# Performance work log

Hardware: AMD Instinct MI355X
Metric: run time of the kernel (lower is better)

Reference implementation:

```python
import jax, jax.numpy as jnp
import numpy as np

B = 64; IMG = 224; P = 16; CIN = 3
DM = 192; DEPTH = 24; DSTATE = 16; DINNER = 384; DTR = 12; DCONV = 4
N = (IMG // P) ** 2  # 196 tokens


def setup_inputs() -> dict:
    key = jax.random.key(0)
    ks = jax.random.split(key, 10)
    s = 0.02
    img = jax.random.normal(ks[0], (B, CIN, IMG, IMG), jnp.float32)
    patch_w = jax.random.normal(ks[1], (DM, CIN, P, P), jnp.float32) * s
    patch_b = jnp.zeros((DM,), jnp.float32)
    # per-layer Mamba params, stacked along depth
    in_proj_w = jax.random.normal(ks[2], (DEPTH, 2 * DINNER, DM), jnp.float32) * s
    conv_w = jax.random.normal(ks[3], (DEPTH, DINNER, DCONV), jnp.float32) * s
    conv_b = jnp.zeros((DEPTH, DINNER), jnp.float32)
    x_proj_w = jax.random.normal(ks[4], (DEPTH, DTR + 2 * DSTATE, DINNER), jnp.float32) * s
    dt_w = jax.random.normal(ks[5], (DEPTH, DINNER, DTR), jnp.float32) * s
    dt_b = jax.random.normal(ks[6], (DEPTH, DINNER), jnp.float32) * s
    # S4D-real init: A = -[1..d_state]
    A_log = jnp.log(jnp.broadcast_to(jnp.arange(1, DSTATE + 1, dtype=jnp.float32), (DEPTH, DINNER, DSTATE)))
    D_param = jnp.ones((DEPTH, DINNER), jnp.float32)
    out_proj_w = jax.random.normal(ks[7], (DEPTH, DM, DINNER), jnp.float32) * s
    norm_w = jnp.ones((DM,), jnp.float32)
    norm_b = jnp.zeros((DM,), jnp.float32)
    return dict(img=img, patch_w=patch_w, patch_b=patch_b, in_proj_w=in_proj_w,
                conv_w=conv_w, conv_b=conv_b, x_proj_w=x_proj_w, dt_w=dt_w, dt_b=dt_b,
                A_log=A_log, D_param=D_param, out_proj_w=out_proj_w,
                norm_w=norm_w, norm_b=norm_b)


def _mamba(x, p):
    # x: (B, L, DM); one Mamba mixer block (mamba_ssm semantics, no residual)
    in_w, cw, cb, xpw, dtw, dtb, A_log, Dv, outw = p
    Bb, L, _ = x.shape
    xz = jnp.einsum('bld,ed->ble', x, in_w)          # (B,L,2*DINNER)
    xs, z = jnp.split(xz, 2, axis=-1)
    # causal depthwise conv1d, kernel size DCONV
    xpad = jnp.pad(xs, ((0, 0), (DCONV - 1, 0), (0, 0)))
    xc = cb + sum(xpad[:, k:k + L, :] * cw[:, k] for k in range(DCONV))
    xc = jax.nn.silu(xc)
    proj = jnp.einsum('bld,ed->ble', xc, xpw)        # (B,L,DTR+2*DSTATE)
    dt = jax.nn.softplus(jnp.einsum('blr,dr->bld', proj[..., :DTR], dtw) + dtb)  # (B,L,DINNER)
    Bm = proj[..., DTR:DTR + DSTATE]                 # (B,L,DSTATE)
    Cm = proj[..., DTR + DSTATE:]                    # (B,L,DSTATE)
    A = -jnp.exp(A_log)                              # (DINNER,DSTATE)

    def step(h, inp):
        dt_t, B_t, u_t, C_t = inp                    # (B,DINNER),(B,DSTATE),(B,DINNER),(B,DSTATE)
        dA = jnp.exp(dt_t[:, :, None] * A)
        h = h * dA + dt_t[:, :, None] * B_t[:, None, :] * u_t[:, :, None]
        y = jnp.einsum('bds,bs->bd', h, C_t)
        return h, y

    h0 = jnp.zeros((Bb, DINNER, DSTATE), x.dtype)
    _, ys = jax.lax.scan(step, h0, (dt.transpose(1, 0, 2), Bm.transpose(1, 0, 2),
                                    xc.transpose(1, 0, 2), Cm.transpose(1, 0, 2)))
    y = ys.transpose(1, 0, 2) + xc * Dv
    y = y * jax.nn.silu(z)
    return jnp.einsum('bld,od->blo', y, outw)


def _forward(img, patch_w, patch_b, in_proj_w, conv_w, conv_b, x_proj_w, dt_w, dt_b,
             A_log, D_param, out_proj_w, norm_w, norm_b):
    x = jax.lax.conv_general_dilated(img, patch_w, (P, P), 'VALID',
                                     dimension_numbers=('NCHW', 'OIHW', 'NCHW'))
    x = x + patch_b[None, :, None, None]
    x = x.reshape(x.shape[0], DM, N).transpose(0, 2, 1)  # (B,N,DM)

    def layer(c, p):
        return _mamba(c, p), None

    x, _ = jax.lax.scan(layer, x, (in_proj_w, conv_w, conv_b, x_proj_w, dt_w, dt_b,
                                   A_log, D_param, out_proj_w))
    mu = x.mean(-1, keepdims=True)
    var = ((x - mu) ** 2).mean(-1, keepdims=True)
    x = (x - mu) / jnp.sqrt(var + 1e-5) * norm_w + norm_b
    return x.mean(axis=1)  # pooled (B, DM)


def reference(img, patch_w, patch_b, in_proj_w, conv_w, conv_b, x_proj_w, dt_w, dt_b,
              A_log, D_param, out_proj_w, norm_w, norm_b):
    return _forward(img, patch_w, patch_b, in_proj_w, conv_w, conv_b, x_proj_w,
                    dt_w, dt_b, A_log, D_param, out_proj_w, norm_w, norm_b)
```

## Files before the change

kernel.cpp:

```cpp
#include <hip/hip_runtime.h>
#include <hip/hip_bf16.h>
#include <math.h>

#define BB 64
#define IMG 224
#define PP 16
#define CIN 3
#define DM 192
#define DEPTH 24
#define DSTATE 16
#define DINNER 384
#define DTR 12
#define DCONV 4
#define NP 196
#define RTOT (BB * NP)
#define CHUNKS 14
#define LC 14
#define NCMB (2 * DSTATE + DINNER)

typedef short bf16x8 __attribute__((ext_vector_type(8)));
typedef float f32x4 __attribute__((ext_vector_type(4)));

__device__ inline unsigned short f2bf_rne(float f) {
    unsigned u = __float_as_uint(f);
    unsigned r = u + 0x7fffu + ((u >> 16) & 1u);
    return (unsigned short)(r >> 16);
}
__device__ inline float bf2f(unsigned short s) {
    return __uint_as_float(((unsigned)s) << 16);
}

__global__ __launch_bounds__(256) void im2col_pack_kernel(const float* __restrict__ img,
                                                          short* __restrict__ colH) {
    size_t idx = (size_t)blockIdx.x * 256 + threadIdx.x;
    if (idx >= (size_t)RTOT * 768) return;
    int t = (int)(idx % 768);
    size_t r = idx / 768;
    int l = (int)(r % NP);
    int b = (int)(r / NP);
    int ph = l / 14, pw = l % 14;
    int ci = t / 256, rem = t % 256;
    int i = rem / 16, j = rem % 16;
    float v = img[(((size_t)b * CIN + ci) * IMG + ph * 16 + i) * IMG + pw * 16 + j];
    colH[idx] = (short)f2bf_rne(v);
}

__global__ __launch_bounds__(256) void pack_w_kernel(const float* __restrict__ W,
                                                     short* __restrict__ Wh, int NE) {
    int i = blockIdx.x * 256 + threadIdx.x;
    if (i * 4 >= NE) return;
    float4 v = *(const float4*)&W[i * 4];
    short4 h;
    h.x = (short)f2bf_rne(v.x);
    h.y = (short)f2bf_rne(v.y);
    h.z = (short)f2bf_rne(v.z);
    h.w = (short)f2bf_rne(v.w);
    *(short4*)&Wh[i * 4] = h;
}

__global__ __launch_bounds__(256) void packT_out_kernel(const float* __restrict__ outw,
                                                        short* __restrict__ wOutT) {
    int idx = blockIdx.x * 256 + threadIdx.x;
    if (idx >= DEPTH * DM * DINNER) return;
    int layer = idx / (DM * DINNER);
    int rem = idx % (DM * DINNER);
    int m = rem / DINNER;
    int k = rem % DINNER;
    float v = outw[idx];
    wOutT[((size_t)layer * DINNER + k) * DM + m] = (short)f2bf_rne(v);
}

__global__ __launch_bounds__(256) void wcmb_kernel(const float* __restrict__ xpw,
                                                   const float* __restrict__ dtw,
                                                   short* __restrict__ wCmb) {
    int idx = blockIdx.x * 256 + threadIdx.x;
    if (idx >= DEPTH * NCMB * DINNER) return;
    int layer = idx / (NCMB * DINNER);
    int rem = idx % (NCMB * DINNER);
    int n = rem / DINNER;
    int k = rem % DINNER;
    const float* xp = xpw + (size_t)layer * 44 * DINNER;
    float v;
    if (n < 32) {
        v = xp[(DTR + n) * DINNER + k];
    } else {
        int d = n - 32;
        const float* w = dtw + ((size_t)layer * DINNER + d) * DTR;
        v = 0.f;
#pragma unroll
        for (int j = 0; j < DTR; j++) v += w[j] * xp[j * DINNER + k];
    }
    wCmb[idx] = (short)f2bf_rne(v);
}

__global__ __launch_bounds__(256) void gemm_wcross_kernel(const short* __restrict__ wIn,
                                                          const short* __restrict__ wOutT,
                                                          short* __restrict__ wCross) {
    constexpr int BK = 32, LDSS = BK + 8, K = DM;
    __shared__ short As[2][64 * LDSS];
    __shared__ short Bs[2][64 * LDSS];
    const int tid = threadIdx.x;
    const int lane = tid & 63;
    const int wc = tid >> 6;
    const int layer = blockIdx.z;
    const short* Ah = wIn + ((size_t)(layer + 1)) * 768 * DM;
    const short* Bh = wOutT + (size_t)layer * DINNER * DM;
    short* Cc = wCross + (size_t)layer * 768 * DINNER;
    const int row0 = blockIdx.y * 64, col0 = blockIdx.x * 64;

    bf16x8 aPh, bPh;
    f32x4 acc[4] = {};

    auto loadG = [&](int k0) {
        int r = tid >> 2, cg = (tid & 3) * 8;
        aPh = *(const bf16x8*)&Ah[(size_t)(row0 + r) * K + k0 + cg];
        bPh = *(const bf16x8*)&Bh[(size_t)(col0 + r) * K + k0 + cg];
    };
    auto storeLDS = [&](int p) {
        int r = tid >> 2, cg = (tid & 3) * 8;
        *(bf16x8*)&As[p][r * LDSS + cg] = aPh;
        *(bf16x8*)&Bs[p][r * LDSS + cg] = bPh;
    };
    auto compute = [&](int p) {
        const int fr = lane & 15;
        const int kg = (lane >> 4) * 8;
        bf16x8 aH[4], bH;
#pragma unroll
        for (int i = 0; i < 4; i++)
            aH[i] = *(const bf16x8*)&As[p][(i * 16 + fr) * LDSS + kg];
        bH = *(const bf16x8*)&Bs[p][(wc * 16 + fr) * LDSS + kg];
#pragma unroll
        for (int i = 0; i < 4; i++)
            acc[i] = __builtin_amdgcn_mfma_f32_16x16x32_bf16(aH[i], bH, acc[i], 0, 0, 0);
    };

    loadG(0);
    storeLDS(0);
    __syncthreads();
    int p = 0;
    for (int k0 = BK;; k0 += BK) {
        const bool has_next = (k0 < K);
        if (has_next) loadG(k0);
        compute(p);
        if (!has_next) break;
        storeLDS(p ^ 1);
        __syncthreads();
        p ^= 1;
    }

    const int crow = (lane >> 4) * 4;
    const int ccol = lane & 15;
#pragma unroll
    for (int i = 0; i < 4; i++) {
        int gn = col0 + wc * 16 + ccol;
        int gm0 = row0 + i * 16 + crow;
#pragma unroll
        for (int reg = 0; reg < 4; reg++)
            Cc[(size_t)(gm0 + reg) * DINNER + gn] = (short)f2bf_rne(acc[i][reg]);
    }
}

template<int BM, int BN>
__global__ __launch_bounds__(256) void gemm_pk_kernel(const short* __restrict__ Ah,
                                                      const short* __restrict__ Bh,
                                                      float* __restrict__ C,
                                                      short* __restrict__ CBf,
                                                      const float* __restrict__ bias,
                                                      int M, int N, int K, int Kc) {
    constexpr int BK = 32;
    constexpr int LDSS = BK + 8;
    constexpr int WR = BM / 64;
    constexpr int WC = 4 / WR;
    constexpr int NJ = BN / WC / 16;
    constexpr int A8 = BM / 64;
    constexpr int B8 = BN / 64;
    __shared__ short As[2][BM * LDSS];
    __shared__ short Bs[2][BN * LDSS];

    const int tid = threadIdx.x;
    const int lane = tid & 63;
    const int wid = tid >> 6;
    const int wr = wid / WC, wc = wid % WC;
    const int row0 = blockIdx.y * BM, col0 = blockIdx.x * BN;
    const int kbase = blockIdx.z * Kc;
    const bf16x8 ZV = {0, 0, 0, 0, 0, 0, 0, 0};

    bf16x8 aPh[A8], bPh[B8];
    f32x4 acc[4][NJ] = {};

    auto loadG = [&](int k0) {
#pragma unroll
        for (int i = 0; i < A8; i++) {
            int lin = tid + i * 256;
            int r = lin >> 2, cg = (lin & 3) * 8;
            aPh[i] = *(const bf16x8*)&Ah[(size_t)(row0 + r) * K + k0 + cg];
        }
#pragma unroll
        for (int i = 0; i < B8; i++) {
            int lin = tid + i * 256;
            int r = lin >> 2, cg = (lin & 3) * 8;
            int n = col0 + r;
            bPh[i] = (n < N) ? *(const bf16x8*)&Bh[(size_t)n * K + k0 + cg] : ZV;
        }
    };
    auto storeLDS = [&](int p) {
#pragma unroll
        for (int i = 0; i < A8; i++) {
            int lin = tid + i * 256;
            int r = lin >> 2, cg = (lin & 3) * 8;
            *(bf16x8*)&As[p][r * LDSS + cg] = aPh[i];
        }
#pragma unroll
        for (int i = 0; i < B8; i++) {
            int lin = tid + i * 256;
            int r = lin >> 2, cg = (lin & 3) * 8;
            *(bf16x8*)&Bs[p][r * LDSS + cg] = bPh[i];
        }
    };
    auto compute = [&](int p) {
        const int fr = lane & 15;
        const int kg = (lane >> 4) * 8;
        bf16x8 aH[4], bH[NJ];
#pragma unroll
        for (int i = 0; i < 4; i++)
            aH[i] = *(const bf16x8*)&As[p][(wr * 64 + i * 16 + fr) * LDSS + kg];
#pragma unroll
        for (int j = 0; j < NJ; j++)
            bH[j] = *(const bf16x8*)&Bs[p][(wc * (BN / WC) + j * 16 + fr) * LDSS + kg];
#pragma unroll
        for (int i = 0; i < 4; i++)
#pragma unroll
            for (int j = 0; j < NJ; j++)
                acc[i][j] = __builtin_amdgcn_mfma_f32_16x16x32_bf16(aH[i], bH[j], acc[i][j], 0, 0, 0);
    };

    loadG(kbase);
    storeLDS(0);
    __syncthreads();
    int p = 0;
    for (int k0 = kbase + BK;; k0 += BK) {
        const bool has_next = (k0 < kbase + Kc);
        if (has_next) loadG(k0);
        compute(p);
        if (!has_next) break;
        storeLDS(p ^ 1);
        __syncthreads();
        p ^= 1;
    }

    const bool direct = (gridDim.z == 1);
    float* Cout = C + (size_t)blockIdx.z * M * N;
    const int crow = (lane >> 4) * 4;
    const int ccol = lane & 15;
#pragma unroll
    for (int i = 0; i < 4; i++)
#pragma unroll
        for (int j = 0; j < NJ; j++) {
            int gn = col0 + wc * (BN / WC) + j * 16 + ccol;
            if (gn >= N) continue;
            int gm0 = row0 + wr * 64 + i * 16 + crow;
            float bv = (direct && bias) ? bias[gn] : 0.f;
            if (direct && CBf) {
#pragma unroll
                for (int reg = 0; reg < 4; reg++)
                    CBf[(size_t)(gm0 + reg) * N + gn] = (short)f2bf_rne(acc[i][j][reg] + bv);
            } else {
#pragma unroll
                for (int reg = 0; reg < 4; reg++)
                    Cout[(size_t)(gm0 + reg) * N + gn] = acc[i][j][reg] + bv;
            }
        }
}

__global__ __launch_bounds__(256) void gemm_xproj_kernel(const short* __restrict__ Ah,
                                                         const short* __restrict__ Bh,
                                                         float* __restrict__ projBC,
                                                         short* __restrict__ dtB,
                                                         const float* __restrict__ dtb,
                                                         int M, int K) {
    constexpr int BM = 64, BN = 64, BK = 32;
    constexpr int LDSS = BK + 8;
    constexpr int N = NCMB;
    __shared__ short As[2][BM * LDSS];
    __shared__ short Bs[2][BN * LDSS];

    const int tid = threadIdx.x;
    const int lane = tid & 63;
    const int wc = tid >> 6;
    const int row0 = blockIdx.y * BM, col0 = blockIdx.x * BN;
    const bf16x8 ZV = {0, 0, 0, 0, 0, 0, 0, 0};

    bf16x8 aPh, bPh;
    f32x4 acc[4] = {};

    auto loadG = [&](int k0) {
        int r = tid >> 2, cg = (tid & 3) * 8;
        aPh = *(const bf16x8*)&Ah[(size_t)(row0 + r) * K + k0 + cg];
        int n = col0 + r;
        bPh = (n < N) ? *(const bf16x8*)&Bh[(size_t)n * K + k0 + cg] : ZV;
    };
    auto storeLDS = [&](int p) {
        int r = tid >> 2, cg = (tid & 3) * 8;
        *(bf16x8*)&As[p][r * LDSS + cg] = aPh;
        *(bf16x8*)&Bs[p][r * LDSS + cg] = bPh;
    };
    auto compute = [&](int p) {
        const int fr = lane & 15;
        const int kg = (lane >> 4) * 8;
        bf16x8 aH[4], bH;
#pragma unroll
        for (int i = 0; i < 4; i++)
            aH[i] = *(const bf16x8*)&As[p][(i * 16 + fr) * LDSS + kg];
        bH = *(const bf16x8*)&Bs[p][(wc * 16 + fr) * LDSS + kg];
#pragma unroll
        for (int i = 0; i < 4; i++)
            acc[i] = __builtin_amdgcn_mfma_f32_16x16x32_bf16(aH[i], bH, acc[i], 0, 0, 0);
    };

    loadG(0);
    storeLDS(0);
    __syncthreads();
    int p = 0;
    for (int k0 = BK;; k0 += BK) {
        const bool has_next = (k0 < K);
        if (has_next) loadG(k0);
        compute(p);
        if (!has_next) break;
        storeLDS(p ^ 1);
        __syncthreads();
        p ^= 1;
    }

    const int crow = (lane >> 4) * 4;
    const int ccol = lane & 15;
#pragma unroll
    for (int i = 0; i < 4; i++) {
        int gn = col0 + wc * 16 + ccol;
        if (gn >= NCMB) continue;
        int gm0 = row0 + i * 16 + crow;
        if (gn < 32) {
#pragma unroll
            for (int reg = 0; reg < 4; reg++)
                projBC[(size_t)(gm0 + reg) * 32 + gn] = acc[i][reg];
        } else {
            int d = gn - 32;
            float bv = dtb[d];
#pragma unroll
            for (int reg = 0; reg < 4; reg++) {
                float v = acc[i][reg] + bv;
                v = (v > 20.f) ? v : __logf(1.f + __expf(v));
                dtB[(size_t)(gm0 + reg) * DINNER + d] = (short)f2bf_rne(v);
            }
        }
    }
}

__global__ __launch_bounds__(256) void reduce_kernel(const float* __restrict__ parts,
                                                     short* __restrict__ outH,
                                                     const float* __restrict__ bias,
                                                     long MN, int N, int SK) {
    long i = (long)blockIdx.x * 256 + threadIdx.x;
    if (i * 4 >= MN) return;
    float4 acc = *(const float4*)&parts[i * 4];
    for (int z = 1; z < SK; z++) {
        float4 v = *(const float4*)&parts[(size_t)z * MN + i * 4];
        acc.x += v.x; acc.y += v.y; acc.z += v.z; acc.w += v.w;
    }
    if (bias) {
        int col = (int)((i * 4) % N);
        float4 bv = *(const float4*)&bias[col];
        acc.x += bv.x; acc.y += bv.y; acc.z += bv.z; acc.w += bv.w;
    }
    short4 h;
    h.x = (short)f2bf_rne(acc.x);
    h.y = (short)f2bf_rne(acc.y);
    h.z = (short)f2bf_rne(acc.z);
    h.w = (short)f2bf_rne(acc.w);
    *(short4*)&outH[i * 4] = h;
}

__global__ __launch_bounds__(256) void conv_silu_kernel(const short* __restrict__ xzBf,
                                                        const float* __restrict__ cw,
                                                        const float* __restrict__ cb,
                                                        short* __restrict__ xcH) {
    size_t idx = (size_t)blockIdx.x * 256 + threadIdx.x;
    if (idx >= (size_t)RTOT * (DINNER / 4)) return;
    int e0 = (int)(idx % (DINNER / 4)) * 4;
    size_t r = idx / (DINNER / 4);
    int l = (int)(r % NP);
    size_t b = r / NP;
    float acc[4];
    {
        float4 cbv = *(const float4*)&cb[e0];
        acc[0] = cbv.x; acc[1] = cbv.y; acc[2] = cbv.z; acc[3] = cbv.w;
    }
    float4 wv[4];
#pragma unroll
    for (int j = 0; j < 4; j++) wv[j] = *(const float4*)&cw[(e0 + j) * DCONV];
#pragma unroll
    for (int k = 0; k < DCONV; k++) {
        int ls = l + k - (DCONV - 1);
        if (ls >= 0) {
            short4 xv = *(const short4*)&xzBf[(b * NP + ls) * 768 + e0];
            acc[0] += bf2f((unsigned short)xv.x) * (&wv[0].x)[k];
            acc[1] += bf2f((unsigned short)xv.y) * (&wv[1].x)[k];
            acc[2] += bf2f((unsigned short)xv.z) * (&wv[2].x)[k];
            acc[3] += bf2f((unsigned short)xv.w) * (&wv[3].x)[k];
        }
    }
    short4 o;
#pragma unroll
    for (int j = 0; j < 4; j++) {
        float v = acc[j] / (1.f + __expf(-acc[j]));
        (&o.x)[j] = (short)f2bf_rne(v);
    }
    *(short4*)&xcH[r * DINNER + e0] = o;
}

__global__ __launch_bounds__(128) void scanA_kernel(const short* __restrict__ xcB,
                                                    const float* __restrict__ projBC,
                                                    const short* __restrict__ dtB,
                                                    const float* __restrict__ A_log,
                                                    float* __restrict__ hEnd,
                                                    float* __restrict__ prodDA) {
    int d = blockIdx.x * 128 + threadIdx.x;
    int c = blockIdx.y, b = blockIdx.z;
    float a[DSTATE], h[DSTATE];
#pragma unroll
    for (int s = 0; s < DSTATE; s++) {
        a[s] = -expf(A_log[(size_t)d * DSTATE + s]);
        h[s] = 0.f;
    }
    const float a0 = a[0];
    bool chain = true;
#pragma unroll
    for (int s = 1; s < DSTATE; s++)
        chain = chain && (fabsf(a[s] - (float)(s + 1) * a0) <= 1e-4f * fabsf(a[s]));
    float sdt = 0.f;
    size_t rbase = (size_t)b * NP + (size_t)c * LC;
    if (chain) {
        for (int l = 0; l < LC; l++) {
            size_t r = rbase + l;
            float dtv = bf2f((unsigned short)dtB[r * DINNER + d]);
            float du = dtv * bf2f((unsigned short)xcB[r * DINNER + d]);
            const float* pb = projBC + r * 32;
            float Bv[DSTATE];
            *(float4*)&Bv[0]  = *(const float4*)&pb[0];
            *(float4*)&Bv[4]  = *(const float4*)&pb[4];
            *(float4*)&Bv[8]  = *(const float4*)&pb[8];
            *(float4*)&Bv[12] = *(const float4*)&pb[12];
            float q = __expf(dtv * a0);
            float dA = q;
            h[0] = h[0] * dA + du * Bv[0];
#pragma unroll
            for (int s = 1; s < DSTATE; s++) {
                dA *= q;
                h[s] = h[s] * dA + du * Bv[s];
            }
            sdt += dtv;
        }
    } else {
        for (int l = 0; l < LC; l++) {
            size_t r = rbase + l;
            float dtv = bf2f((unsigned short)dtB[r * DINNER + d]);
            float du = dtv * bf2f((unsigned short)xcB[r * DINNER + d]);
            const float* pb = projBC + r * 32;
            float Bv[DSTATE];
            *(float4*)&Bv[0]  = *(const float4*)&pb[0];
            *(float4*)&Bv[4]  = *(const float4*)&pb[4];
            *(float4*)&Bv[8]  = *(const float4*)&pb[8];
            *(float4*)&Bv[12] = *(const float4*)&pb[12];
#pragma unroll
            for (int s = 0; s < DSTATE; s++) {
                float dA = __expf(dtv * a[s]);
                h[s] = h[s] * dA + du * Bv[s];
            }
            sdt += dtv;
        }
    }
    float* he = hEnd   + (((size_t)b * CHUNKS + c) * DINNER + d) * DSTATE;
    float* pd = prodDA + (((size_t)b * CHUNKS + c) * DINNER + d) * DSTATE;
#pragma unroll
    for (int g = 0; g < 4; g++)
        *(float4*)&he[g * 4] = *(float4*)&h[g * 4];
    float pv[DSTATE];
#pragma unroll
    for (int s = 0; s < DSTATE; s++) pv[s] = __expf(a[s] * sdt);
#pragma unroll
    for (int g = 0; g < 4; g++)
        *(float4*)&pd[g * 4] = *(float4*)&pv[g * 4];
}

__global__ __launch_bounds__(256) void scanB_kernel(const float* __restrict__ hEnd,
                                                    float* __restrict__ prodDA) {
    int idx = blockIdx.x * 256 + threadIdx.x;
    if (idx >= BB * DINNER * DSTATE) return;
    int b = idx / (DINNER * DSTATE);
    int rem = idx % (DINNER * DSTATE);
    float run = 0.f;
    for (int c = 0; c < CHUNKS; c++) {
        size_t off = ((size_t)b * CHUNKS + c) * (DINNER * DSTATE) + rem;
        float p = prodDA[off];
        float e = hEnd[off];
        prodDA[off] = run;
        run = run * p + e;
    }
}

__global__ __launch_bounds__(128) void scanC_kernel(const short* __restrict__ xcB,
                                                    const float* __restrict__ projBC,
                                                    const short* __restrict__ dtB,
                                                    const float* __restrict__ hInit,
                                                    const float* __restrict__ A_log,
                                                    const float* __restrict__ Dv,
                                                    const short* __restrict__ xzBf,
                                                    short* __restrict__ yh) {
    int d = blockIdx.x * 128 + threadIdx.x;
    int c = blockIdx.y, b = blockIdx.z;
    float a[DSTATE], h[DSTATE];
#pragma unroll
    for (int s = 0; s < DSTATE; s++)
        a[s] = -expf(A_log[(size_t)d * DSTATE + s]);
    const float a0 = a[0];
    bool chain = true;
#pragma unroll
    for (int s = 1; s < DSTATE; s++)
        chain = chain && (fabsf(a[s] - (float)(s + 1) * a0) <= 1e-4f * fabsf(a[s]));
    const float* hi = hInit + (((size_t)b * CHUNKS + c) * DINNER + d) * DSTATE;
#pragma unroll
    for (int g = 0; g < 4; g++)
        *(float4*)&h[g * 4] = *(const float4*)&hi[g * 4];
    float Dd = Dv[d];
    size_t rbase = (size_t)b * NP + (size_t)c * LC;
    if (chain) {
        for (int l = 0; l < LC; l++) {
            size_t r = rbase + l;
            float dtv = bf2f((unsigned short)dtB[r * DINNER + d]);
            float u = bf2f((unsigned short)xcB[r * DINNER + d]);
            float du = dtv * u;
            const float* pb = projBC + r * 32;
            float Bv[DSTATE], Cv[DSTATE];
            *(float4*)&Bv[0]  = *(const float4*)&pb[0];
            *(float4*)&Bv[4]  = *(const float4*)&pb[4];
            *(float4*)&Bv[8]  = *(const float4*)&pb[8];
            *(float4*)&Bv[12] = *(const float4*)&pb[12];
            *(float4*)&Cv[0]  = *(const float4*)&pb[16];
            *(float4*)&Cv[4]  = *(const float4*)&pb[20];
            *(float4*)&Cv[8]  = *(const float4*)&pb[24];
            *(float4*)&Cv[12] = *(const float4*)&pb[28];
            float q = __expf(dtv * a0);
            float dA = q;
            h[0] = h[0] * dA + du * Bv[0];
            float y = h[0] * Cv[0];
#pragma unroll
            for (int s = 1; s < DSTATE; s++) {
                dA *= q;
                h[s] = h[s] * dA + du * Bv[s];
                y = fmaf(h[s], Cv[s], y);
            }
            float z = bf2f((unsigned short)xzBf[r * 768 + DINNER + d]);
            float val = (y + u * Dd) * (z / (1.f + __expf(-z)));
            yh[r * DINNER + d] = (short)f2bf_rne(val);
        }
    } else {
        for (int l = 0; l < LC; l++) {
            size_t r = rbase + l;
            float dtv = bf2f((unsigned short)dtB[r * DINNER + d]);
            float u = bf2f((unsigned short)xcB[r * DINNER + d]);
            float du = dtv * u;
            const float* pb = projBC + r * 32;
            float Bv[DSTATE], Cv[DSTATE];
            *(float4*)&Bv[0]  = *(const float4*)&pb[0];
            *(float4*)&Bv[4]  = *(const float4*)&pb[4];
            *(float4*)&Bv[8]  = *(const float4*)&pb[8];
            *(float4*)&Bv[12] = *(const float4*)&pb[12];
            *(float4*)&Cv[0]  = *(const float4*)&pb[16];
            *(float4*)&Cv[4]  = *(const float4*)&pb[20];
            *(float4*)&Cv[8]  = *(const float4*)&pb[24];
            *(float4*)&Cv[12] = *(const float4*)&pb[28];
            float y = 0.f;
#pragma unroll
            for (int s = 0; s < DSTATE; s++) {
                float dA = __expf(dtv * a[s]);
                h[s] = h[s] * dA + du * Bv[s];
                y = fmaf(h[s], Cv[s], y);
            }
            float z = bf2f((unsigned short)xzBf[r * 768 + DINNER + d]);
            float val = (y + u * Dd) * (z / (1.f + __expf(-z)));
            yh[r * DINNER + d] = (short)f2bf_rne(val);
        }
    }
}

__global__ __launch_bounds__(256) void ln_stats_kernel(const short* __restrict__ xh,
                                                       float* __restrict__ stats) {
    int r = blockIdx.x * 4 + (threadIdx.x >> 6);
    int lane = threadIdx.x & 63;
    if (r >= RTOT) return;
    float s = 0.f, ss = 0.f;
    for (int c = lane; c < DM; c += 64) {
        float v = bf2f((unsigned short)xh[(size_t)r * DM + c]);
        s += v;
        ss += v * v;
    }
#pragma unroll
    for (int o = 32; o > 0; o >>= 1) {
        s += __shfl_down(s, o);
        ss += __shfl_down(ss, o);
    }
    if (lane == 0) {
        float mu = s / (float)DM;
        float var = ss / (float)DM - mu * mu;
        stats[r * 2] = mu;
        stats[r * 2 + 1] = rsqrtf(var + 1e-5f);
    }
}

__global__ __launch_bounds__(256) void ln_mean_kernel(const short* __restrict__ xh,
                                                      const float* __restrict__ stats,
                                                      const float* __restrict__ nw,
                                                      const float* __restrict__ nb,
                                                      float* __restrict__ out) {
    int idx = blockIdx.x * 256 + threadIdx.x;
    if (idx >= BB * DM) return;
    int c = idx % DM;
    int b = idx / DM;
    float acc = 0.f;
    for (int l = 0; l < NP; l++) {
        size_t r = (size_t)b * NP + l;
        float v = bf2f((unsigned short)xh[r * DM + c]);
        acc += (v - stats[r * 2]) * stats[r * 2 + 1];
    }
    out[idx] = acc * (1.f / (float)NP) * nw[c] + nb[c];
}

extern "C" void kernel_launch(void* const* d_in, const int* in_sizes, int n_in,
                              void* d_out, int out_size, void* d_ws, size_t ws_size,
                              hipStream_t stream) {
    const float* img     = (const float*)d_in[0];
    const float* patch_w = (const float*)d_in[1];
    const float* patch_b = (const float*)d_in[2];
    const float* in_w    = (const float*)d_in[3];
    const float* conv_w  = (const float*)d_in[4];
    const float* conv_b  = (const float*)d_in[5];
    const float* xpw     = (const float*)d_in[6];
    const float* dtw     = (const float*)d_in[7];
    const float* dtb     = (const float*)d_in[8];
    const float* A_log   = (const float*)d_in[9];
    const float* Dv      = (const float*)d_in[10];
    const float* outw    = (const float*)d_in[11];
    const float* norm_w  = (const float*)d_in[12];
    const float* norm_b  = (const float*)d_in[13];
    float* out = (float*)d_out;

    float* ws = (float*)d_ws;
    const size_t R = RTOT;
    const size_t SCN = (size_t)BB * CHUNKS * DINNER * DSTATE;

    float* xA      = ws;
    float* xB      = xA + R * DM / 2;
    float* xzB     = xB + R * DM / 2;
    float* xcB     = xzB + R * 768 / 2;
    float* dtBf    = xcB + R * DINNER / 2;
    float* projBC  = dtBf + R * DINNER / 2;
    float* scratch = projBC + R * 32;
    float* wAll    = scratch + 2 * SCN;
    float* wCrossF = wAll + 4644864;
    float* stats   = wCrossF + 3391488;

    short* wPatch = (short*)wAll;
    short* wIn    = wPatch + (size_t)DM * 768;
    short* wOut   = wIn + (size_t)DEPTH * 2 * DINNER * DM;
    short* wCmb   = wOut + (size_t)DEPTH * DM * DINNER;
    short* wCross = (short*)wCrossF;

    short* y2h = (short*)scratch;
    short* wOutT = (short*)scratch;

    pack_w_kernel<<<dim3((DM * 768 / 4 + 255) / 256), 256, 0, stream>>>(
        patch_w, wPatch, DM * 768);
    pack_w_kernel<<<dim3((DEPTH * 2 * DINNER * DM / 4 + 255) / 256), 256, 0, stream>>>(
        in_w, wIn, DEPTH * 2 * DINNER * DM);
    pack_w_kernel<<<dim3((DEPTH * DM * DINNER / 4 + 255) / 256), 256, 0, stream>>>(
        outw, wOut, DEPTH * DM * DINNER);
    wcmb_kernel<<<dim3((DEPTH * NCMB * DINNER + 255) / 256), 256, 0, stream>>>(
        xpw, dtw, wCmb);
    packT_out_kernel<<<dim3((DEPTH * DM * DINNER + 255) / 256), 256, 0, stream>>>(
        outw, wOutT);
    gemm_wcross_kernel<<<dim3(DINNER / 64, 768 / 64, DEPTH - 1), 256, 0, stream>>>(
        wIn, wOutT, wCross);

    {
        short* colH = (short*)xzB;
        size_t n = R * 768;
        im2col_pack_kernel<<<dim3((unsigned)((n + 255) / 256)), 256, 0, stream>>>(img, colH);
        gemm_pk_kernel<64, 64><<<dim3(3, RTOT / 64, 4), 256, 0, stream>>>(
            colH, wPatch, scratch, nullptr, nullptr, RTOT, DM, 768, 192);
        long MN = (long)RTOT * DM;
        reduce_kernel<<<dim3((unsigned)((MN / 4 + 255) / 256)), 256, 0, stream>>>(
            scratch, (short*)xA, patch_b, MN, DM, 4);
    }

    short* xzH = (short*)xzB;
    short* xcH = (short*)xcB;
    short* dtH = (short*)dtBf;

    gemm_pk_kernel<64, 128><<<dim3(768 / 128, RTOT / 64, 1), 256, 0, stream>>>(
        (short*)xA, wIn, nullptr, xzH, nullptr, RTOT, 2 * DINNER, DM, DM);

    for (int layer = 0; layer < DEPTH; layer++) {
        const float* conv_wl = conv_w + (size_t)layer * DINNER * DCONV;
        const float* conv_bl = conv_b + (size_t)layer * DINNER;
        const float* dtb_l   = dtb + (size_t)layer * DINNER;
        const float* Alog_l  = A_log + (size_t)layer * DINNER * DSTATE;
        const float* Dv_l    = Dv + (size_t)layer * DINNER;
        short* wCmb_l = wCmb + (size_t)layer * NCMB * DINNER;

        {
            size_t n = R * (DINNER / 4);
            conv_silu_kernel<<<dim3((unsigned)((n + 255) / 256)), 256, 0, stream>>>(
                xzH, conv_wl, conv_bl, xcH);
        }
        gemm_xproj_kernel<<<dim3(7, RTOT / 64), 256, 0, stream>>>(
            xcH, wCmb_l, projBC, dtH, dtb_l, RTOT, DINNER);
        scanA_kernel<<<dim3(3, CHUNKS, BB), 128, 0, stream>>>(
            xcH, projBC, dtH, Alog_l, scratch, scratch + SCN);
        scanB_kernel<<<dim3((BB * DINNER * DSTATE + 255) / 256), 256, 0, stream>>>(
            scratch, scratch + SCN);
        scanC_kernel<<<dim3(3, CHUNKS, BB), 128, 0, stream>>>(
            xcH, projBC, dtH, scratch + SCN, Alog_l, Dv_l, xzH, y2h);
        if (layer < DEPTH - 1) {
            short* wX = wCross + (size_t)layer * 768 * DINNER;
            gemm_pk_kernel<64, 128><<<dim3(768 / 128, RTOT / 64, 1), 256, 0, stream>>>(
                y2h, wX, nullptr, xzH, nullptr, RTOT, 2 * DINNER, DINNER, DINNER);
        } else {
            short* wOut_l = wOut + (size_t)layer * DM * DINNER;
            gemm_pk_kernel<64, 64><<<dim3(DM / 64, RTOT / 64, 1), 256, 0, stream>>>(
                y2h, wOut_l, nullptr, (short*)xB, nullptr, RTOT, DM, DINNER, DINNER);
        }
    }

    short* xfH = (short*)xB;
    ln_stats_kernel<<<dim3(RTOT / 4), 256, 0, stream>>>(xfH, stats);
    ln_mean_kernel<<<dim3((BB * DM + 255) / 256), 256, 0, stream>>>(
        xfH, stats, norm_w, norm_b, out);
}
```

Measured before the change: 2.901 ms.

## Store chunk scan states in bf16 and recompute decay products from chunk dt sums

The chunked selective scan now writes each chunk's end states as bf16 instead of fp32. It also stores one per-channel dt sum per chunk instead of a full per-state decay product array, and scanB recomputes each decay with exp. The carried-in states passed to scanC are likewise bf16. This cuts the inter-kernel traffic of the three scan passes by roughly half or more, at the cost of precision loss in the carried state and some extra exp work in scanB.

After: 2.568 ms. -11.5%, faster.

```diff
diff --git a/kernel.cpp b/kernel.cpp
--- a/kernel.cpp
+++ b/kernel.cpp
@@ -421,8 +421,8 @@
                                                     const float* __restrict__ projBC,
                                                     const short* __restrict__ dtB,
                                                     const float* __restrict__ A_log,
-                                                    float* __restrict__ hEnd,
-                                                    float* __restrict__ prodDA) {
+                                                    short* __restrict__ hEndB,
+                                                    float* __restrict__ sdtBuf) {
     int d = blockIdx.x * 128 + threadIdx.x;
     int c = blockIdx.y, b = blockIdx.z;
     float a[DSTATE], h[DSTATE];
@@ -478,31 +478,36 @@
             sdt += dtv;
         }
     }
-    float* he = hEnd   + (((size_t)b * CHUNKS + c) * DINNER + d) * DSTATE;
-    float* pd = prodDA + (((size_t)b * CHUNKS + c) * DINNER + d) * DSTATE;
-#pragma unroll
-    for (int g = 0; g < 4; g++)
-        *(float4*)&he[g * 4] = *(float4*)&h[g * 4];
-    float pv[DSTATE];
-#pragma unroll
-    for (int s = 0; s < DSTATE; s++) pv[s] = __expf(a[s] * sdt);
-#pragma unroll
-    for (int g = 0; g < 4; g++)
-        *(float4*)&pd[g * 4] = *(float4*)&pv[g * 4];
-}
-
-__global__ __launch_bounds__(256) void scanB_kernel(const float* __restrict__ hEnd,
-                                                    float* __restrict__ prodDA) {
+    short* he = hEndB + (((size_t)b * CHUNKS + c) * DINNER + d) * DSTATE;
+#pragma unroll
+    for (int g = 0; g < 4; g++) {
+        short4 o;
+        o.x = (short)f2bf_rne(h[g * 4 + 0]);
+        o.y = (short)f2bf_rne(h[g * 4 + 1]);
+        o.z = (short)f2bf_rne(h[g * 4 + 2]);
+        o.w = (short)f2bf_rne(h[g * 4 + 3]);
+        *(short4*)&he[g * 4] = o;
+    }
+    sdtBuf[((size_t)b * CHUNKS + c) * DINNER + d] = sdt;
+}
+
+__global__ __launch_bounds__(256) void scanB_kernel(const short* __restrict__ hEndB,
+                                                    const float* __restrict__ sdtBuf,
+                                                    const float* __restrict__ A_log,
+                                                    short* __restrict__ hInitB) {
     int idx = blockIdx.x * 256 + threadIdx.x;
     if (idx >= BB * DINNER * DSTATE) return;
     int b = idx / (DINNER * DSTATE);
     int rem = idx % (DINNER * DSTATE);
+    int d = rem / DSTATE;
+    int s = rem % DSTATE;
+    float a = -expf(A_log[(size_t)d * DSTATE + s]);
     float run = 0.f;
     for (int c = 0; c < CHUNKS; c++) {
         size_t off = ((size_t)b * CHUNKS + c) * (DINNER * DSTATE) + rem;
-        float p = prodDA[off];
-        float e = hEnd[off];
-        prodDA[off] = run;
+        float p = __expf(a * sdtBuf[((size_t)b * CHUNKS + c) * DINNER + d]);
+        float e = bf2f((unsigned short)hEndB[off]);
+        hInitB[off] = (short)f2bf_rne(run);
         run = run * p + e;
     }
 }
@@ -510,7 +515,7 @@
 __global__ __launch_bounds__(128) void scanC_kernel(const short* __restrict__ xcB,
                                                     const float* __restrict__ projBC,
                                                     const short* __restrict__ dtB,
-                                                    const float* __restrict__ hInit,
+                                                    const short* __restrict__ hInitB,
                                                     const float* __restrict__ A_log,
                                                     const float* __restrict__ Dv,
                                                     const short* __restrict__ xzBf,
@@ -526,10 +531,15 @@
 #pragma unroll
     for (int s = 1; s < DSTATE; s++)
         chain = chain && (fabsf(a[s] - (float)(s + 1) * a0) <= 1e-4f * fabsf(a[s]));
-    const float* hi = hInit + (((size_t)b * CHUNKS + c) * DINNER + d) * DSTATE;
-#pragma unroll
-    for (int g = 0; g < 4; g++)
-        *(float4*)&h[g * 4] = *(const float4*)&hi[g * 4];
+    const short* hi = hInitB + (((size_t)b * CHUNKS + c) * DINNER + d) * DSTATE;
+#pragma unroll
+    for (int g = 0; g < 4; g++) {
+        short4 v = *(const short4*)&hi[g * 4];
+        h[g * 4 + 0] = bf2f((unsigned short)v.x);
+        h[g * 4 + 1] = bf2f((unsigned short)v.y);
+        h[g * 4 + 2] = bf2f((unsigned short)v.z);
+        h[g * 4 + 3] = bf2f((unsigned short)v.w);
+    }
     float Dd = Dv[d];
     size_t rbase = (size_t)b * NP + (size_t)c * LC;
     if (chain) {
@@ -656,6 +666,7 @@
     float* ws = (float*)d_ws;
     const size_t R = RTOT;
     const size_t SCN = (size_t)BB * CHUNKS * DINNER * DSTATE;
+    const size_t PLY = R * DINNER;
 
     float* xA      = ws;
     float* xB      = xA + R * DM / 2;
@@ -674,8 +685,11 @@
     short* wCmb   = wOut + (size_t)DEPTH * DM * DINNER;
     short* wCross = (short*)wCrossF;
 
-    short* y2h = (short*)scratch;
-    short* wOutT = (short*)scratch;
+    short* hEndB  = (short*)scratch;
+    short* hInitB = hEndB + SCN;
+    float* sdtBuf = scratch + SCN;
+    short* y2h    = (short*)(sdtBuf + (size_t)BB * CHUNKS * DINNER);
+    short* wOutT  = (short*)scratch;
 
     pack_w_kernel<<<dim3((DM * 768 / 4 + 255) / 256), 256, 0, stream>>>(
         patch_w, wPatch, DM * 768);
@@ -724,11 +738,11 @@
         gemm_xproj_kernel<<<dim3(7, RTOT / 64), 256, 0, stream>>>(
             xcH, wCmb_l, projBC, dtH, dtb_l, RTOT, DINNER);
         scanA_kernel<<<dim3(3, CHUNKS, BB), 128, 0, stream>>>(
-            xcH, projBC, dtH, Alog_l, scratch, scratch + SCN);
+            xcH, projBC, dtH, Alog_l, hEndB, sdtBuf);
         scanB_kernel<<<dim3((BB * DINNER * DSTATE + 255) / 256), 256, 0, stream>>>(
-            scratch, scratch + SCN);
+            hEndB, sdtBuf, Alog_l, hInitB);
         scanC_kernel<<<dim3(3, CHUNKS, BB), 128, 0, stream>>>(
-            xcH, projBC, dtH, scratch + SCN, Alog_l, Dv_l, xzH, y2h);
+            xcH, projBC, dtH, hInitB, Alog_l, Dv_l, xzH, y2h);
         if (layer < DEPTH - 1) {
             short* wX = wCross + (size_t)layer * 768 * DINNER;
             gemm_pk_kernel<64, 128><<<dim3(768 / 128, RTOT / 64, 1), 256, 0, stream>>>(
```
